# Kernel optimization log

Hardware: AMD Instinct MI355X
Metric: run time of the kernel (lower is better)

Reference implementation:

```python
import jax, jax.numpy as jnp
import numpy as np

B, H, N, HD = 8, 12, 577, 64   # batch, heads, tokens (576 patches + CLS), head dim
GRID = 24                      # 384 / 16
TEMP = 0.1                     # RelaxedBernoulli temperature
EPS = 1e-6


def _make_dists():
    # pairwise (row,col) offsets between patch grid positions, CLS row/col padded with 0
    r, c = np.indices((GRID, GRID))
    idx = np.stack([r.ravel(), c.ravel()], axis=-1).astype(np.float32)   # (576, 2)
    d = idx[:, None, :] - idx[None, :, :]                                # (576, 576, 2)
    d = np.pad(d, ((1, 0), (1, 0), (0, 0)))                              # (577, 577, 2)
    return jnp.asarray(d)


def setup_inputs() -> dict:
    key = jax.random.key(0)
    kq, k1, k2, ku = jax.random.split(key, 4)
    return {
        "query": jax.random.normal(kq, (B, H, N, HD), dtype=jnp.float32),
        "W1": jax.random.normal(k1, (HD, 64), dtype=jnp.float32) * 0.02,
        "b1": jnp.zeros((64,), dtype=jnp.float32),
        "W2": jax.random.normal(k2, (64, 3), dtype=jnp.float32) * 0.02,
        "b2": jnp.zeros((3,), dtype=jnp.float32),
        "u": jax.random.uniform(ku, (B, H, N, N), dtype=jnp.float32,
                                minval=EPS, maxval=1.0 - EPS),
        "dists": _make_dists(),
    }


def reference(query, W1, b1, W2, b2, u, dists):
    # sigma MLP: Linear -> gelu -> Linear  ->  (b,h,n,3)
    s = jax.nn.gelu(query @ W1 + b1, approximate=False) @ W2 + b2

    # per-token 2x2 covariance: [[sx^2, rho*sx*sy], [rho*sx*sy, sy^2]]
    sx = jax.nn.relu(s[..., 0]) + 1.0
    sy = jax.nn.relu(s[..., 1]) + 1.0
    rho = 0.99 * jnp.tanh(s[..., 2])
    sxx = sx * sx
    syy = sy * sy
    sxy = rho * sx * sy

    # closed-form 2x2 inverse
    det = sxx * syy - sxy * sxy
    inv00 = syy / det
    inv11 = sxx / det
    inv01 = -sxy / det

    # quadratic form d^T Sinv d without materializing (b,h,n,n,2,2)
    dx = dists[..., 0]   # (n, n)
    dy = dists[..., 1]
    w = -0.5 * (jnp.einsum('bhi,ij->bhij', inv00, dx * dx)
                + 2.0 * jnp.einsum('bhi,ij->bhij', inv01, dx * dy)
                + jnp.einsum('bhi,ij->bhij', inv11, dy * dy))

    kernel = jnp.exp(w)
    probs = kernel / jnp.max(kernel, axis=-1, keepdims=True)
    probs = jnp.clip(probs, EPS, 1.0 - EPS)

    # RelaxedBernoulli reparameterized sample with logistic noise from u
    logits = jnp.log(probs) - jnp.log1p(-probs)
    noise = jnp.log(u) - jnp.log1p(-u)
    mask = jax.nn.sigmoid((logits + noise) / TEMP)
    return mask
```

## Files before the change

kernel.cpp:

```cpp
#include <hip/hip_runtime.h>
#include <math.h>

#define BHN    55392
#define NTOK   577
#define HD     64
#define EPS_F  1e-6f
#define ROWS_PER_BLOCK 4
#define NBLOCKS (BHN / ROWS_PER_BLOCK)
#define VEC_PER_BLOCK 577

typedef float v4f __attribute__((ext_vector_type(4)));

__global__ __launch_bounds__(256) void fused_mask_kernel(
    const float*  __restrict__ q,  const float* __restrict__ W1,
    const float*  __restrict__ b1, const float* __restrict__ W2,
    const float*  __restrict__ b2, const v4f* __restrict__ u4,
    v4f* __restrict__ out4)
{
    __shared__ float4 coef_s[ROWS_PER_BLOCK];

    const int tid  = threadIdx.x;
    const int lane = tid & 63;
    const int wv   = tid >> 6;
    const int tok  = blockIdx.x * ROWS_PER_BLOCK + wv;

    {
        const float* qrow = q + (size_t)tok * HD;
        float h = 0.0f;
        #pragma unroll 8
        for (int k = 0; k < HD; ++k)
            h = fmaf(qrow[k], W1[k * HD + lane], h);

        float x = h + b1[lane];
        float z  = x * 0.70710678118654752f;
        float az = fabsf(z);
        float kk = __builtin_amdgcn_rcpf(fmaf(0.3275911f, az, 1.0f));
        float poly = kk * (0.254829592f + kk * (-0.284496736f +
                     kk * (1.421413741f + kk * (-1.453152027f +
                     kk * 1.061405429f))));
        float om   = poly * __expf(-z * z);
        float erfz = copysignf(1.0f - om, z);
        float g = 0.5f * x * (1.0f + erfz);

        float s0 = g * W2[lane * 3 + 0];
        float s1 = g * W2[lane * 3 + 1];
        float s2 = g * W2[lane * 3 + 2];

        #pragma unroll
        for (int off = 1; off < 64; off <<= 1) {
            s0 += __shfl_xor(s0, off);
            s1 += __shfl_xor(s1, off);
            s2 += __shfl_xor(s2, off);
        }

        if (lane == 0) {
            s0 += b2[0]; s1 += b2[1]; s2 += b2[2];
            float sx = fmaxf(s0, 0.0f) + 1.0f;
            float sy = fmaxf(s1, 0.0f) + 1.0f;
            float ex = __expf(2.0f * s2);
            float rho = 0.99f * ((ex - 1.0f) * __builtin_amdgcn_rcpf(ex + 1.0f));
            float sxx = sx * sx, syy = sy * sy;
            float sxy = rho * sx * sy;
            float det = sxx * syy - sxy * sxy;
            float inv_det = 1.0f / det;

            float a = -0.5f * syy * inv_det;
            float b =  sxy * inv_det;
            float c = -0.5f * sxx * inv_det;

            int i = tok % NTOK;
            float pack;
            if (i == 0) { a = 0.0f; b = 0.0f; c = 0.0f; pack = 0.0f; }
            else {
                int ip = i - 1;
                int ri = ip / 24;
                int ci = ip - ri * 24;
                pack = (float)(ri * 32 + ci);
            }
            coef_s[wv] = make_float4(a, b, c, pack);
        }
    }
    __syncthreads();

    const float4 c0 = coef_s[0];
    const float4 c1 = coef_s[1];
    const float4 c2 = coef_s[2];
    const float4 c3 = coef_s[3];

    const size_t base = (size_t)blockIdx.x * VEC_PER_BLOCK;

    #pragma unroll 1
    for (int it = tid; it < VEC_PER_BLOCK; it += 256) {
        v4f uu = __builtin_nontemporal_load(&u4[base + it]);
        float um[4] = {uu.x, uu.y, uu.z, uu.w};
        float res[4];

        int e0 = it * 4;
        #pragma unroll
        for (int m = 0; m < 4; ++m) {
            int e = e0 + m;
            int rl = (e >= 1731) ? 3 : ((e >= 1154) ? 2 : ((e >= 577) ? 1 : 0));
            int j  = e - rl * 577;
            float4 cf = (rl == 0) ? c0 : ((rl == 1) ? c1 : ((rl == 2) ? c2 : c3));
            int rc = (int)cf.w;

            float dx = 0.0f, dy = 0.0f;
            if (j > 0) {
                unsigned jj = (unsigned)(j - 1);
                unsigned rj = jj / 24u;
                unsigned cj = jj - rj * 24u;
                dx = (float)((rc >> 5) - (int)rj);
                dy = (float)((rc & 31) - (int)cj);
            }

            float w = fmaf(fmaf(cf.x, dx, cf.y * dy), dx, cf.z * (dy * dy));

            float p = __expf(w);
            p = fminf(fmaxf(p, EPS_F), 1.0f - EPS_F);

            float uk  = um[m];
            float num = p * uk;
            float den = (1.0f - p) * (1.0f - uk);
            float r   = den * __builtin_amdgcn_rcpf(num);

            float r2  = r * r;
            float r4  = r2 * r2;
            float r5  = r4 * r;
            float r10 = r5 * r5;

            res[m] = __builtin_amdgcn_rcpf(1.0f + r10);
        }

        v4f o = {res[0], res[1], res[2], res[3]};
        __builtin_nontemporal_store(o, &out4[base + it]);
    }
}

extern "C" void kernel_launch(void* const* d_in, const int* in_sizes, int n_in,
                              void* d_out, int out_size, void* d_ws, size_t ws_size,
                              hipStream_t stream) {
    const float* q  = (const float*)d_in[0];
    const float* W1 = (const float*)d_in[1];
    const float* b1 = (const float*)d_in[2];
    const float* W2 = (const float*)d_in[3];
    const float* b2 = (const float*)d_in[4];
    const float* u  = (const float*)d_in[5];

    fused_mask_kernel<<<NBLOCKS, 256, 0, stream>>>(
        q, W1, b1, W2, b2, (const v4f*)u, (v4f*)d_out);
}
```

Before: 284.7 us.

## Process one row per wavefront, dropping shared memory and block barrier

Each wavefront now computes its own token's covariance coefficients redundantly in every lane and streams its own 577-element row with scalar loads and stores. This removes the shared-memory handoff, the __syncthreads, and the per-element row-selection logic. The exponential becomes exp2 with log2(e) folded into the coefficients. The cost is scalar 4-byte accesses in place of 16-byte vector ones, since rows are not 16-byte aligned, plus a serial tail element handled by lane 0.

```diff
diff --git a/kernel.cpp b/kernel.cpp
--- a/kernel.cpp
+++ b/kernel.cpp
@@ -5,134 +5,128 @@
 #define NTOK   577
 #define HD     64
 #define EPS_F  1e-6f
-#define ROWS_PER_BLOCK 4
-#define NBLOCKS (BHN / ROWS_PER_BLOCK)
-#define VEC_PER_BLOCK 577
+#define NBLOCKS (BHN / 4)
 
-typedef float v4f __attribute__((ext_vector_type(4)));
+#if __has_builtin(__builtin_amdgcn_exp2f)
+#define EXP2F __builtin_amdgcn_exp2f
+#else
+#define EXP2F exp2f
+#endif
 
 __global__ __launch_bounds__(256) void fused_mask_kernel(
-    const float*  __restrict__ q,  const float* __restrict__ W1,
-    const float*  __restrict__ b1, const float* __restrict__ W2,
-    const float*  __restrict__ b2, const v4f* __restrict__ u4,
-    v4f* __restrict__ out4)
+    const float* __restrict__ q,  const float* __restrict__ W1,
+    const float* __restrict__ b1, const float* __restrict__ W2,
+    const float* __restrict__ b2, const float* __restrict__ u,
+    float* __restrict__ out)
 {
-    __shared__ float4 coef_s[ROWS_PER_BLOCK];
-
     const int tid  = threadIdx.x;
     const int lane = tid & 63;
-    const int wv   = tid >> 6;
-    const int tok  = blockIdx.x * ROWS_PER_BLOCK + wv;
+    const int tok  = blockIdx.x * 4 + (tid >> 6);
 
-    {
-        const float* qrow = q + (size_t)tok * HD;
-        float h = 0.0f;
-        #pragma unroll 8
-        for (int k = 0; k < HD; ++k)
-            h = fmaf(qrow[k], W1[k * HD + lane], h);
+    const float* qrow = q + (size_t)tok * HD;
+    float h = 0.0f;
+    #pragma unroll 8
+    for (int k = 0; k < HD; ++k)
+        h = fmaf(qrow[k], W1[k * HD + lane], h);
 
-        float x = h + b1[lane];
-        float z  = x * 0.70710678118654752f;
-        float az = fabsf(z);
-        float kk = __builtin_amdgcn_rcpf(fmaf(0.3275911f, az, 1.0f));
-        float poly = kk * (0.254829592f + kk * (-0.284496736f +
-                     kk * (1.421413741f + kk * (-1.453152027f +
-                     kk * 1.061405429f))));
-        float om   = poly * __expf(-z * z);
-        float erfz = copysignf(1.0f - om, z);
-        float g = 0.5f * x * (1.0f + erfz);
+    float x = h + b1[lane];
+    float z  = x * 0.70710678118654752f;
+    float az = fabsf(z);
+    float kk = __builtin_amdgcn_rcpf(fmaf(0.3275911f, az, 1.0f));
+    float poly = kk * (0.254829592f + kk * (-0.284496736f +
+                 kk * (1.421413741f + kk * (-1.453152027f +
+                 kk * 1.061405429f))));
+    float om   = poly * __expf(-z * z);
+    float erfz = copysignf(1.0f - om, z);
+    float g = 0.5f * x * (1.0f + erfz);
 
-        float s0 = g * W2[lane * 3 + 0];
-        float s1 = g * W2[lane * 3 + 1];
-        float s2 = g * W2[lane * 3 + 2];
+    float s0 = g * W2[lane * 3 + 0];
+    float s1 = g * W2[lane * 3 + 1];
+    float s2 = g * W2[lane * 3 + 2];
 
-        #pragma unroll
-        for (int off = 1; off < 64; off <<= 1) {
-            s0 += __shfl_xor(s0, off);
-            s1 += __shfl_xor(s1, off);
-            s2 += __shfl_xor(s2, off);
-        }
+    #pragma unroll
+    for (int off = 1; off < 64; off <<= 1) {
+        s0 += __shfl_xor(s0, off);
+        s1 += __shfl_xor(s1, off);
+        s2 += __shfl_xor(s2, off);
+    }
+    s0 += b2[0]; s1 += b2[1]; s2 += b2[2];
 
-        if (lane == 0) {
-            s0 += b2[0]; s1 += b2[1]; s2 += b2[2];
-            float sx = fmaxf(s0, 0.0f) + 1.0f;
-            float sy = fmaxf(s1, 0.0f) + 1.0f;
-            float ex = __expf(2.0f * s2);
-            float rho = 0.99f * ((ex - 1.0f) * __builtin_amdgcn_rcpf(ex + 1.0f));
-            float sxx = sx * sx, syy = sy * sy;
-            float sxy = rho * sx * sy;
-            float det = sxx * syy - sxy * sxy;
-            float inv_det = 1.0f / det;
+    float sx = fmaxf(s0, 0.0f) + 1.0f;
+    float sy = fmaxf(s1, 0.0f) + 1.0f;
+    float ex = __expf(2.0f * s2);
+    float rho = 0.99f * ((ex - 1.0f) * __builtin_amdgcn_rcpf(ex + 1.0f));
+    float sxx = sx * sx, syy = sy * sy;
+    float sxy = rho * sx * sy;
+    float det = sxx * syy - sxy * sxy;
+    float inv_s = 1.4426950408889634f / det;
 
-            float a = -0.5f * syy * inv_det;
-            float b =  sxy * inv_det;
-            float c = -0.5f * sxx * inv_det;
+    float ca = -0.5f * syy * inv_s;
+    float cb =  sxy * inv_s;
+    float cc = -0.5f * sxx * inv_s;
 
-            int i = tok % NTOK;
-            float pack;
-            if (i == 0) { a = 0.0f; b = 0.0f; c = 0.0f; pack = 0.0f; }
-            else {
-                int ip = i - 1;
-                int ri = ip / 24;
-                int ci = ip - ri * 24;
-                pack = (float)(ri * 32 + ci);
-            }
-            coef_s[wv] = make_float4(a, b, c, pack);
-        }
+    const int i = tok % NTOK;
+    float rif, cif;
+    if (i == 0) {
+        ca = 0.0f; cb = 0.0f; cc = 0.0f; rif = 0.0f; cif = 0.0f;
+    } else {
+        int ip = i - 1;
+        int ri = ip / 24;
+        int ci = ip - ri * 24;
+        rif = (float)ri; cif = (float)ci;
     }
-    __syncthreads();
 
-    const float4 c0 = coef_s[0];
-    const float4 c1 = coef_s[1];
-    const float4 c2 = coef_s[2];
-    const float4 c3 = coef_s[3];
+    const float* urow = u   + (size_t)tok * NTOK;
+    float*       orow = out + (size_t)tok * NTOK;
 
-    const size_t base = (size_t)blockIdx.x * VEC_PER_BLOCK;
+    int j = lane;
+    #pragma unroll 1
+    for (int step = 0; step < 9; ++step, j += 64) {
+        float uk = urow[j];
 
-    #pragma unroll 1
-    for (int it = tid; it < VEC_PER_BLOCK; it += 256) {
-        v4f uu = __builtin_nontemporal_load(&u4[base + it]);
-        float um[4] = {uu.x, uu.y, uu.z, uu.w};
-        float res[4];
+        unsigned jj = (unsigned)(j - 1);
+        unsigned rj = jj / 24u;
+        unsigned cj = jj - rj * 24u;
+        float dx = rif - (float)rj;
+        float dy = cif - (float)cj;
+        if (j == 0) { dx = 0.0f; dy = 0.0f; }
 
-        int e0 = it * 4;
-        #pragma unroll
-        for (int m = 0; m < 4; ++m) {
-            int e = e0 + m;
-            int rl = (e >= 1731) ? 3 : ((e >= 1154) ? 2 : ((e >= 577) ? 1 : 0));
-            int j  = e - rl * 577;
-            float4 cf = (rl == 0) ? c0 : ((rl == 1) ? c1 : ((rl == 2) ? c2 : c3));
-            int rc = (int)cf.w;
+        float w = fmaf(fmaf(ca, dx, cb * dy), dx, cc * (dy * dy));
 
-            float dx = 0.0f, dy = 0.0f;
-            if (j > 0) {
-                unsigned jj = (unsigned)(j - 1);
-                unsigned rj = jj / 24u;
-                unsigned cj = jj - rj * 24u;
-                dx = (float)((rc >> 5) - (int)rj);
-                dy = (float)((rc & 31) - (int)cj);
-            }
+        float p = EXP2F(w);
+        p = fminf(fmaxf(p, EPS_F), 1.0f - EPS_F);
 
-            float w = fmaf(fmaf(cf.x, dx, cf.y * dy), dx, cf.z * (dy * dy));
+        float num = p * uk;
+        float den = (1.0f - p) * (1.0f - uk);
+        float r   = den * __builtin_amdgcn_rcpf(num);
 
-            float p = __expf(w);
-            p = fminf(fmaxf(p, EPS_F), 1.0f - EPS_F);
+        float r2  = r * r;
+        float r4  = r2 * r2;
+        float r5  = r4 * r;
+        float r10 = r5 * r5;
 
-            float uk  = um[m];
-            float num = p * uk;
-            float den = (1.0f - p) * (1.0f - uk);
-            float r   = den * __builtin_amdgcn_rcpf(num);
+        float res = __builtin_amdgcn_rcpf(1.0f + r10);
+        __builtin_nontemporal_store(res, &orow[j]);
+    }
 
-            float r2  = r * r;
-            float r4  = r2 * r2;
-            float r5  = r4 * r;
-            float r10 = r5 * r5;
-
-            res[m] = __builtin_amdgcn_rcpf(1.0f + r10);
-        }
-
-        v4f o = {res[0], res[1], res[2], res[3]};
-        __builtin_nontemporal_store(o, &out4[base + it]);
+    if (lane == 0) {
+        float uk = urow[576];
+        unsigned jj = 575u;
+        unsigned rj = jj / 24u;
+        unsigned cj = jj - rj * 24u;
+        float dx = rif - (float)rj;
+        float dy = cif - (float)cj;
+        float w = fmaf(fmaf(ca, dx, cb * dy), dx, cc * (dy * dy));
+        float p = EXP2F(w);
+        p = fminf(fmaxf(p, EPS_F), 1.0f - EPS_F);
+        float num = p * uk;
+        float den = (1.0f - p) * (1.0f - uk);
+        float r   = den * __builtin_amdgcn_rcpf(num);
+        float r2  = r * r;
+        float r4  = r2 * r2;
+        float r10 = r4 * r4 * r2;
+        float res = __builtin_amdgcn_rcpf(1.0f + r10);
+        __builtin_nontemporal_store(res, &orow[576]);
     }
 }
 
@@ -147,5 +141,5 @@
     const float* u  = (const float*)d_in[5];
 
     fused_mask_kernel<<<NBLOCKS, 256, 0, stream>>>(
-        q, W1, b1, W2, b2, (const v4f*)u, (v4f*)d_out);
+        q, W1, b1, W2, b2, u, (float*)d_out);
 }
```

Result: slower. 303.8 us (+6.7%).
